# Kernel optimization log

Hardware: AMD Instinct MI355X
Metric: run time of the kernel (lower is better)

## Reference

```python
import jax, jax.numpy as jnp
import numpy as np

HEADS = 16

def setup_inputs() -> dict:
    key = jax.random.key(0)
    k1, k2, k3 = jax.random.split(key, 3)
    B, S, D = 2, 2048, 1024
    return {
        "query": jax.random.normal(k1, (B, S, D), dtype=jnp.float32),
        "key": jax.random.normal(k2, (B, S, D), dtype=jnp.float32),
        "value": jax.random.normal(k3, (B, S, D), dtype=jnp.float32),
    }

def reference(query, key, value):
    B, S, D = query.shape
    H = HEADS
    dh = D // H
    # split(-1) into H equal chunks == reshape to (B, S, H, dh)
    q = query.reshape(B, S, H, dh)
    k = key.reshape(B, S, H, dh)
    v = value.reshape(B, S, H, dh)
    scale = 1.0 / jnp.sqrt(jnp.asarray(dh, dtype=query.dtype))
    scores = jnp.einsum('bqhd,bkhd->bhqk', q, k) * scale  # [B,H,S,S]
    probs = jax.nn.softmax(scores, axis=-1)
    out = jnp.einsum('bhqk,bkhd->bqhd', probs, v)  # [B,S,H,dh]
    return out.reshape(B, S, D)
```

## Files before the change

### kernel.cpp

```cpp
#include <hip/hip_runtime.h>
#include <stdint.h>


#define B_ 2
#define S_ 2048
#define D_ 1024
#define H_ 16
#define DH 64
#define M_TILE 128
#define N_TILE 128
#define NITER (S_ / N_TILE)

typedef __bf16 bf16;
typedef __bf16 bf16x2 __attribute__((ext_vector_type(2)));
typedef __bf16 bf16x4 __attribute__((ext_vector_type(4)));
typedef __bf16 bf16x8 __attribute__((ext_vector_type(8)));
typedef float floatx4 __attribute__((ext_vector_type(4)));

#define KB_TOTAL (B_ * S_ * D_ * 2)
#define KROW_B (D_ * 2)
#define KB_HEAD (S_ * DH * 2)
#define VT_ROW (S_ * 2)
#define WS_NEEDED (2u * KB_TOTAL)

#define N_TILE2 64
#define NITER2 (S_ / N_TILE2)
#define KT2 8192
#define BUF2 16384
#define LSH_OFF2 (4 * BUF2)
#define SMEM_MAIN (LSH_OFF2 + 512)
#define O_STRIDE 36

__device__ __forceinline__ float fast_exp2(float x) {
#if __has_builtin(__builtin_amdgcn_exp2f)
  return __builtin_amdgcn_exp2f(x);
#else
  return exp2f(x);
#endif
}

__device__ __forceinline__ void gl_lds16(const void* g, void* l) {
  __builtin_amdgcn_global_load_lds(
      (const __attribute__((address_space(1))) unsigned int*)g,
      (__attribute__((address_space(3))) unsigned int*)l, 16, 0, 0);
}

__global__ __launch_bounds__(256)
void prep(const float* __restrict__ Kg, const float* __restrict__ Vg,
          unsigned char* __restrict__ ws) {
  const int bid = blockIdx.x;
  const int tid = threadIdx.x;
  if (bid < 512) {
    __shared__ __align__(16) bf16 VTsh[64][136];
    const int head_lin = bid & 31, ktile = bid >> 5;
    const int b = head_lin >> 4, h = head_lin & 15;
    const int kb = ktile * 128;
    const int vr0 = (tid >> 3) << 2;
    const int vf0 = (tid & 7) << 3;
    const float* Vbase = Vg + (size_t)(b * S_) * D_ + h * DH;
    float vals[4][8];
#pragma unroll
    for (int rr = 0; rr < 4; ++rr) {
      const float* vp = Vbase + (size_t)(kb + vr0 + rr) * D_ + vf0;
      float4 a = *(const float4*)vp;
      float4 c = *(const float4*)(vp + 4);
      vals[rr][0] = a.x; vals[rr][1] = a.y; vals[rr][2] = a.z; vals[rr][3] = a.w;
      vals[rr][4] = c.x; vals[rr][5] = c.y; vals[rr][6] = c.z; vals[rr][7] = c.w;
    }
    const int pbase = (vr0 & 96) + ((vr0 >> 2) & 3) * 8 + ((vr0 >> 4) & 1) * 4;
    const int psw = (((pbase >> 3) ^ (tid & 7)) << 3) | (pbase & 7);
#pragma unroll
    for (int j = 0; j < 8; ++j) {
      bf16x4 y = {(bf16)vals[0][j], (bf16)vals[1][j], (bf16)vals[2][j], (bf16)vals[3][j]};
      *(bf16x4*)(&VTsh[vf0 + j][psw]) = y;
    }
    __syncthreads();
    unsigned char* Vout = ws + KB_TOTAL + (size_t)head_lin * KB_HEAD;
#pragma unroll
    for (int j = 0; j < 4; ++j) {
      const int id  = j * 256 + tid;
      const int c   = id & 63;
      const int sub = id >> 6;
      const int fg  = sub & 3;
      const int ckl = sub >> 2;
      const int col = c & 15, quad = c >> 4;
      const int f = fg * 16 + col;
      const int g = ckl * 4 + quad;
      const int gs = g ^ ((f >> 3) & 7);
      bf16x8 v = *(const bf16x8*)(&VTsh[f][gs << 3]);
      *(bf16x8*)(Vout + (size_t)f * VT_ROW + kb * 2 + (ckl * 64 + quad * 16)) = v;
    }
  } else {
    const int idx = (bid - 512) * 256 + tid;
    const float* src = Kg + (size_t)idx * 8;
    float4 x0 = ((const float4*)src)[0];
    float4 x1 = ((const float4*)src)[1];
    bf16x8 y = {(bf16)x0.x, (bf16)x0.y, (bf16)x0.z, (bf16)x0.w,
                (bf16)x1.x, (bf16)x1.y, (bf16)x1.z, (bf16)x1.w};
    *(bf16x8*)(ws + (size_t)idx * 16) = y;
  }
}

__global__ __launch_bounds__(512, 4)
void attn_fwd(const float* __restrict__ Qg, const unsigned char* __restrict__ Kb,
              const unsigned char* __restrict__ VT, float* __restrict__ Og) {
  __shared__ __align__(16) unsigned char smem[SMEM_MAIN];
  float* Osh = (float*)smem;
  float* Lsh = (float*)(smem + LSH_OFF2);

  const int tid  = threadIdx.x;
  const int lane = tid & 63;
  const int wave = tid >> 6;
  const int kw   = wave & 1;
  const int qw   = wave >> 1;
  const int col  = lane & 15;
  const int quad = lane >> 4;

  const int bid      = blockIdx.x;
  const int head_lin = bid & 31;
  const int qtile    = bid >> 5;
  const int b        = head_lin >> 4;
  const int h        = head_lin & 15;

  const unsigned char* Khead = Kb + (size_t)(b * S_) * KROW_B + h * (DH * 2);
  const unsigned char* Vhead = VT + (size_t)head_lin * (DH * VT_ROW);

  const float QSCALE = 0.125f * 1.44269504088896340736f;

  bf16x8 Qf[2][2];
#pragma unroll
  for (int qt = 0; qt < 2; ++qt) {
    const float* base = Qg + (size_t)(b * S_ + qtile * M_TILE + qw * 32 + qt * 16 + col) * D_
                        + h * DH + quad * 8;
#pragma unroll
    for (int ks = 0; ks < 2; ++ks) {
      float4 x0 = *(const float4*)(base + ks * 32);
      float4 x1 = *(const float4*)(base + ks * 32 + 4);
      bf16x8 f;
      f[0] = (bf16)(x0.x * QSCALE); f[1] = (bf16)(x0.y * QSCALE);
      f[2] = (bf16)(x0.z * QSCALE); f[3] = (bf16)(x0.w * QSCALE);
      f[4] = (bf16)(x1.x * QSCALE); f[5] = (bf16)(x1.y * QSCALE);
      f[6] = (bf16)(x1.z * QSCALE); f[7] = (bf16)(x1.w * QSCALE);
      Qf[qt][ks] = f;
    }
  }

  floatx4 accO[4][2];
  float l_lane[2] = {0.f, 0.f};
#pragma unroll
  for (int ft = 0; ft < 4; ++ft)
#pragma unroll
    for (int qt = 0; qt < 2; ++qt) accO[ft][qt] = (floatx4)0.f;

  const int sub = lane >> 3;
  const int gx  = ((lane & 7) ^ sub) << 4;

  auto dma_tile2 = [&](int kbk, int bufoff) {
    const int r = (wave << 3) + sub;
    gl_lds16(Khead + (size_t)(kbk + r) * KROW_B + gx,
             smem + bufoff + (wave << 10));
    gl_lds16(Vhead + (size_t)r * VT_ROW + kbk * 2 + gx,
             smem + bufoff + KT2 + (wave << 10));
  };

  const int cq = col & 7;
  const int ka0_off = (kw * 32 + col) * 128 + ((quad ^ cq) << 4);
  const int ka1_off = (kw * 32 + col) * 128 + (((quad | 4) ^ cq) << 4);
  const int va0_off = KT2 + col * 128 + (((kw * 4 + quad) ^ cq) << 4);

  dma_tile2(0, 0);
  dma_tile2(N_TILE2, BUF2);

  bf16x8 Pf[2];

  for (int it = 0; it < NITER2; ++it) {
    if (it + 2 < NITER2) dma_tile2((it + 2) * N_TILE2, ((it + 2) & 3) * BUF2);
    const int bc = (it & 3) * BUF2;
    const int bp = ((it - 1) & 3) * BUF2;

    __builtin_amdgcn_sched_barrier(0);
    if (it + 2 < NITER2)       asm volatile("s_waitcnt vmcnt(4)" ::: "memory");
    else if (it + 2 == NITER2) asm volatile("s_waitcnt vmcnt(2)" ::: "memory");
    else                       asm volatile("s_waitcnt vmcnt(0)" ::: "memory");
    __builtin_amdgcn_s_barrier();
    asm volatile("" ::: "memory");
    __builtin_amdgcn_sched_barrier(0);

    floatx4 accS[2][2];
    __builtin_amdgcn_s_setprio(1);
#pragma unroll
    for (int kt = 0; kt < 2; ++kt) {
      bf16x8 Ka0 = *(const bf16x8*)(smem + bc + ka0_off + kt * 2048);
      bf16x8 Ka1 = *(const bf16x8*)(smem + bc + ka1_off + kt * 2048);
#pragma unroll
      for (int qt = 0; qt < 2; ++qt) {
        floatx4 a = (floatx4)0.f;
        a = __builtin_amdgcn_mfma_f32_16x16x32_bf16(Ka0, Qf[qt][0], a, 0, 0, 0);
        a = __builtin_amdgcn_mfma_f32_16x16x32_bf16(Ka1, Qf[qt][1], a, 0, 0, 0);
        accS[kt][qt] = a;
      }
    }

    if (it > 0) {
#pragma unroll
      for (int ft = 0; ft < 4; ++ft) {
        bf16x8 Va = *(const bf16x8*)(smem + bp + va0_off + ft * 2048);
#pragma unroll
        for (int qt = 0; qt < 2; ++qt)
          accO[ft][qt] = __builtin_amdgcn_mfma_f32_16x16x32_bf16(Va, Pf[qt], accO[ft][qt], 0, 0, 0);
      }
    }
    __builtin_amdgcn_s_setprio(0);

#pragma unroll
    for (int qt = 0; qt < 2; ++qt) {
      float rs = 0.f;
#pragma unroll
      for (int kt = 0; kt < 2; ++kt)
#pragma unroll
        for (int r = 0; r < 4; ++r) {
          float p = fast_exp2(accS[kt][qt][r]);
          accS[kt][qt][r] = p;
          rs += p;
        }
      l_lane[qt] += rs;
    }
#pragma unroll
    for (int qt = 0; qt < 2; ++qt) {
      floatx4 p0 = accS[0][qt], p1 = accS[1][qt];
      bf16x8 f = {(bf16)p0[0], (bf16)p0[1], (bf16)p0[2], (bf16)p0[3],
                  (bf16)p1[0], (bf16)p1[1], (bf16)p1[2], (bf16)p1[3]};
      Pf[qt] = f;
    }

    __builtin_amdgcn_sched_barrier(0);
    asm volatile("" ::: "memory");
    __builtin_amdgcn_s_barrier();
  }

  {
    const int bp = ((NITER2 - 1) & 3) * BUF2;
    __builtin_amdgcn_s_setprio(1);
#pragma unroll
    for (int ft = 0; ft < 4; ++ft) {
      bf16x8 Va = *(const bf16x8*)(smem + bp + va0_off + ft * 2048);
#pragma unroll
      for (int qt = 0; qt < 2; ++qt)
        accO[ft][qt] = __builtin_amdgcn_mfma_f32_16x16x32_bf16(Va, Pf[qt], accO[ft][qt], 0, 0, 0);
    }
    __builtin_amdgcn_s_setprio(0);
  }
  __syncthreads();

  float l_red[2];
#pragma unroll
  for (int qt = 0; qt < 2; ++qt) {
    float s = l_lane[qt];
    s += __shfl_xor(s, 16);
    s += __shfl_xor(s, 32);
    l_red[qt] = s;
  }

  if (kw == 1) {
    float* r = Osh + (qw * 64 + lane) * O_STRIDE;
#pragma unroll
    for (int qt = 0; qt < 2; ++qt)
#pragma unroll
      for (int ft = 0; ft < 4; ++ft)
        *(floatx4*)(r + (qt * 4 + ft) * 4) = accO[ft][qt];
    if (quad == 0) {
#pragma unroll
      for (int qt = 0; qt < 2; ++qt)
        Lsh[qw * 32 + qt * 16 + col] = l_red[qt];
    }
  }
  __syncthreads();

  if (kw == 0) {
    const float* r = Osh + (qw * 64 + lane) * O_STRIDE;
    float rl[2];
#pragma unroll
    for (int qt = 0; qt < 2; ++qt)
      rl[qt] = 1.0f / (l_red[qt] + Lsh[qw * 32 + qt * 16 + col]);
#pragma unroll
    for (int qt = 0; qt < 2; ++qt) {
      const int q = qtile * M_TILE + qw * 32 + qt * 16 + col;
      float* dst = Og + (size_t)(b * S_ + q) * D_ + h * DH + quad * 4;
#pragma unroll
      for (int ft = 0; ft < 4; ++ft) {
        floatx4 o = (accO[ft][qt] + *(const floatx4*)(r + (qt * 4 + ft) * 4)) * rl[qt];
        *(floatx4*)(dst + ft * 16) = o;
      }
    }
  }
}

#define FB_K_STRIDE 68
#define FB_V_STRIDE 132
#define FB_K_BYTES (128 * FB_K_STRIDE * 2)
#define FB_V_BYTES (64 * FB_V_STRIDE * 2)
#define FB_SMEM ((256 * O_STRIDE * 4 + 2048) > (FB_K_BYTES + FB_V_BYTES) ? (256 * O_STRIDE * 4 + 2048) : (FB_K_BYTES + FB_V_BYTES))

__device__ __forceinline__ bf16x8 cat8(bf16x4 a, bf16x4 b) {
  return __builtin_shufflevector(a, b, 0, 1, 2, 3, 4, 5, 6, 7);
}

__global__ __launch_bounds__(512, 4)
void attn_fwd_fb(const float* __restrict__ Qg, const float* __restrict__ Kg,
                 const float* __restrict__ Vg, float* __restrict__ Og) {
  __shared__ __align__(16) unsigned char smem[FB_SMEM];
  bf16*  Ksh = (bf16*)smem;
  bf16*  Vsh = (bf16*)(smem + FB_K_BYTES);
  float* Osh = (float*)smem;
  float* Lsh = (float*)(smem + 256 * O_STRIDE * 4);

  const int tid  = threadIdx.x;
  const int lane = tid & 63;
  const int wave = tid >> 6;
  const int kw   = wave & 1;
  const int qw   = wave >> 1;
  const int col  = lane & 15;
  const int quad = lane >> 4;
  const int bid      = blockIdx.x;
  const int head_lin = bid & 31;
  const int qtile    = bid >> 5;
  const int b        = head_lin >> 4;
  const int h        = head_lin & 15;
  const float QSCALE = 0.125f * 1.44269504088896340736f;

  bf16x8 Qf[2][2];
#pragma unroll
  for (int qt = 0; qt < 2; ++qt) {
    const float* base = Qg + (size_t)(b * S_ + qtile * 128 + qw * 32 + qt * 16 + col) * D_
                        + h * DH + quad * 8;
#pragma unroll
    for (int ks = 0; ks < 2; ++ks) {
      float4 x0 = *(const float4*)(base + ks * 32);
      float4 x1 = *(const float4*)(base + ks * 32 + 4);
      bf16x8 f;
      f[0] = (bf16)(x0.x * QSCALE); f[1] = (bf16)(x0.y * QSCALE);
      f[2] = (bf16)(x0.z * QSCALE); f[3] = (bf16)(x0.w * QSCALE);
      f[4] = (bf16)(x1.x * QSCALE); f[5] = (bf16)(x1.y * QSCALE);
      f[6] = (bf16)(x1.z * QSCALE); f[7] = (bf16)(x1.w * QSCALE);
      Qf[qt][ks] = f;
    }
  }

  floatx4 accO[4][2];
  float l_lane[2] = {0.f, 0.f};
#pragma unroll
  for (int ft = 0; ft < 4; ++ft)
#pragma unroll
    for (int qt = 0; qt < 2; ++qt) accO[ft][qt] = (floatx4)0.f;

  const float* Kbase = Kg + (size_t)(b * S_) * D_ + h * DH;
  const float* Vbase = Vg + (size_t)(b * S_) * D_ + h * DH;
  const int krow0 = tid >> 4;
  const int kf4   = tid & 15;
  const int vk0   = (tid >> 3) * 2;
  const int vf0   = (tid & 7) * 8;

  for (int it = 0; it < NITER; ++it) {
    const int kb = it * 128;
    float4 kx[4];
#pragma unroll
    for (int i = 0; i < 4; ++i)
      kx[i] = *(const float4*)(Kbase + (size_t)(kb + krow0 + 32 * i) * D_ + kf4 * 4);
    float4 va0 = *(const float4*)(Vbase + (size_t)(kb + vk0) * D_ + vf0);
    float4 va1 = *(const float4*)(Vbase + (size_t)(kb + vk0) * D_ + vf0 + 4);
    float4 vb0 = *(const float4*)(Vbase + (size_t)(kb + vk0 + 1) * D_ + vf0);
    float4 vb1 = *(const float4*)(Vbase + (size_t)(kb + vk0 + 1) * D_ + vf0 + 4);
#pragma unroll
    for (int i = 0; i < 4; ++i) {
      bf16x4 y = {(bf16)kx[i].x, (bf16)kx[i].y, (bf16)kx[i].z, (bf16)kx[i].w};
      *(bf16x4*)(Ksh + (krow0 + 32 * i) * FB_K_STRIDE + kf4 * 4) = y;
    }
    {
      float a[8] = {va0.x, va0.y, va0.z, va0.w, va1.x, va1.y, va1.z, va1.w};
      float c[8] = {vb0.x, vb0.y, vb0.z, vb0.w, vb1.x, vb1.y, vb1.z, vb1.w};
#pragma unroll
      for (int j = 0; j < 8; ++j) {
        bf16x2 y = {(bf16)a[j], (bf16)c[j]};
        *(bf16x2*)(Vsh + (vf0 + j) * FB_V_STRIDE + vk0) = y;
      }
    }
    __syncthreads();

    floatx4 accS[4][2];
#pragma unroll
    for (int kt = 0; kt < 4; ++kt) {
      const bf16* kp = Ksh + (kw * 64 + kt * 16 + col) * FB_K_STRIDE + quad * 8;
      bf16x8 Ka0 = cat8(*(const bf16x4*)kp, *(const bf16x4*)(kp + 4));
      bf16x8 Ka1 = cat8(*(const bf16x4*)(kp + 32), *(const bf16x4*)(kp + 36));
#pragma unroll
      for (int qt = 0; qt < 2; ++qt) {
        floatx4 a = (floatx4)0.f;
        a = __builtin_amdgcn_mfma_f32_16x16x32_bf16(Ka0, Qf[qt][0], a, 0, 0, 0);
        a = __builtin_amdgcn_mfma_f32_16x16x32_bf16(Ka1, Qf[qt][1], a, 0, 0, 0);
        accS[kt][qt] = a;
      }
    }
#pragma unroll
    for (int qt = 0; qt < 2; ++qt) {
      float rs = 0.f;
#pragma unroll
      for (int kt = 0; kt < 4; ++kt)
#pragma unroll
        for (int r = 0; r < 4; ++r) {
          float p = fast_exp2(accS[kt][qt][r]);
          accS[kt][qt][r] = p;
          rs += p;
        }
      l_lane[qt] += rs;
    }
#pragma unroll
    for (int c = 0; c < 2; ++c) {
      bf16x8 Pf[2];
#pragma unroll
      for (int qt = 0; qt < 2; ++qt) {
        floatx4 p0 = accS[2 * c][qt], p1 = accS[2 * c + 1][qt];
        bf16x8 f = {(bf16)p0[0], (bf16)p0[1], (bf16)p0[2], (bf16)p0[3],
                    (bf16)p1[0], (bf16)p1[1], (bf16)p1[2], (bf16)p1[3]};
        Pf[qt] = f;
      }
#pragma unroll
      for (int ft = 0; ft < 4; ++ft) {
        const bf16* vp = Vsh + (ft * 16 + col) * FB_V_STRIDE + kw * 64 + 32 * c + quad * 4;
        bf16x8 Va = cat8(*(const bf16x4*)vp, *(const bf16x4*)(vp + 16));
#pragma unroll
        for (int qt = 0; qt < 2; ++qt)
          accO[ft][qt] = __builtin_amdgcn_mfma_f32_16x16x32_bf16(Va, Pf[qt], accO[ft][qt], 0, 0, 0);
      }
    }
    __syncthreads();
  }

  float l_red[2];
#pragma unroll
  for (int qt = 0; qt < 2; ++qt) {
    float s = l_lane[qt];
    s += __shfl_xor(s, 16);
    s += __shfl_xor(s, 32);
    l_red[qt] = s;
  }
  if (kw == 1) {
    float* r = Osh + (qw * 64 + lane) * O_STRIDE;
#pragma unroll
    for (int qt = 0; qt < 2; ++qt)
#pragma unroll
      for (int ft = 0; ft < 4; ++ft)
        *(floatx4*)(r + (qt * 4 + ft) * 4) = accO[ft][qt];
    if (quad == 0) {
#pragma unroll
      for (int qt = 0; qt < 2; ++qt)
        Lsh[qw * 32 + qt * 16 + col] = l_red[qt];
    }
  }
  __syncthreads();
  if (kw == 0) {
    const float* r = Osh + (qw * 64 + lane) * O_STRIDE;
    float rl[2];
#pragma unroll
    for (int qt = 0; qt < 2; ++qt)
      rl[qt] = 1.0f / (l_red[qt] + Lsh[qw * 32 + qt * 16 + col]);
#pragma unroll
    for (int qt = 0; qt < 2; ++qt) {
      const int q = qtile * 128 + qw * 32 + qt * 16 + col;
      float* dst = Og + (size_t)(b * S_ + q) * D_ + h * DH + quad * 4;
#pragma unroll
      for (int ft = 0; ft < 4; ++ft) {
        floatx4 o = (accO[ft][qt] + *(const floatx4*)(r + (qt * 4 + ft) * 4)) * rl[qt];
        *(floatx4*)(dst + ft * 16) = o;
      }
    }
  }
}

extern "C" void kernel_launch(void* const* d_in, const int* in_sizes, int n_in,
                              void* d_out, int out_size, void* d_ws, size_t ws_size,
                              hipStream_t stream) {
  const float* Q = (const float*)d_in[0];
  const float* K = (const float*)d_in[1];
  const float* V = (const float*)d_in[2];
  float* O = (float*)d_out;
  if (ws_size >= WS_NEEDED && d_ws != nullptr) {
    unsigned char* ws = (unsigned char*)d_ws;
    hipLaunchKernelGGL(prep, dim3(2560), dim3(256), 0, stream, K, V, ws);
    hipLaunchKernelGGL(attn_fwd, dim3(B_ * H_ * (S_ / M_TILE)), dim3(512), 0, stream,
                       Q, ws, ws + KB_TOTAL, O);
  } else {
    hipLaunchKernelGGL(attn_fwd_fb, dim3(512), dim3(512), 0, stream, Q, K, V, O);
  }
}
```

Baseline: 128.5 us.

## Load fp32 K directly into LDS and convert in-kernel, drop K prep pass

The separate K fp32-to-bf16 conversion pass is removed from the prep kernel, which now only transposes V. The attention kernel DMAs raw fp32 K rows into LDS, with a swizzle, and converts to bf16 after the LDS read. The pipeline changes from 4 buffers with 2 tiles in flight to 3 larger buffers with 1 tile prefetched. This saves the K write and re-read through the workspace, but each K tile now moves twice the bytes through global memory and LDS, LDS use grows, and prefetch depth shrinks, which may hurt occupancy and latency hiding.

```diff
diff --git a/kernel.cpp b/kernel.cpp
--- a/kernel.cpp
+++ b/kernel.cpp
@@ -17,18 +17,17 @@
 typedef __bf16 bf16x8 __attribute__((ext_vector_type(8)));
 typedef float floatx4 __attribute__((ext_vector_type(4)));
 
-#define KB_TOTAL (B_ * S_ * D_ * 2)
-#define KROW_B (D_ * 2)
 #define KB_HEAD (S_ * DH * 2)
 #define VT_ROW (S_ * 2)
-#define WS_NEEDED (2u * KB_TOTAL)
+#define WS_NEEDED (32u * KB_HEAD)
+#define KROW_RAW 4096
 
 #define N_TILE2 64
 #define NITER2 (S_ / N_TILE2)
-#define KT2 8192
-#define BUF2 16384
-#define LSH_OFF2 (4 * BUF2)
-#define SMEM_MAIN (LSH_OFF2 + 512)
+#define KT3 16384
+#define BUF3 24576
+#define LSH3 (3 * BUF3)
+#define SMEM_MAIN (LSH3 + 512)
 #define O_STRIDE 36
 
 __device__ __forceinline__ float fast_exp2(float x) {
@@ -46,67 +45,56 @@
 }
 
 __global__ __launch_bounds__(256)
-void prep(const float* __restrict__ Kg, const float* __restrict__ Vg,
-          unsigned char* __restrict__ ws) {
+void prep(const float* __restrict__ Vg, unsigned char* __restrict__ ws) {
+  __shared__ __align__(16) bf16 VTsh[64][136];
   const int bid = blockIdx.x;
   const int tid = threadIdx.x;
-  if (bid < 512) {
-    __shared__ __align__(16) bf16 VTsh[64][136];
-    const int head_lin = bid & 31, ktile = bid >> 5;
-    const int b = head_lin >> 4, h = head_lin & 15;
-    const int kb = ktile * 128;
-    const int vr0 = (tid >> 3) << 2;
-    const int vf0 = (tid & 7) << 3;
-    const float* Vbase = Vg + (size_t)(b * S_) * D_ + h * DH;
-    float vals[4][8];
-#pragma unroll
-    for (int rr = 0; rr < 4; ++rr) {
-      const float* vp = Vbase + (size_t)(kb + vr0 + rr) * D_ + vf0;
-      float4 a = *(const float4*)vp;
-      float4 c = *(const float4*)(vp + 4);
-      vals[rr][0] = a.x; vals[rr][1] = a.y; vals[rr][2] = a.z; vals[rr][3] = a.w;
-      vals[rr][4] = c.x; vals[rr][5] = c.y; vals[rr][6] = c.z; vals[rr][7] = c.w;
-    }
-    const int pbase = (vr0 & 96) + ((vr0 >> 2) & 3) * 8 + ((vr0 >> 4) & 1) * 4;
-    const int psw = (((pbase >> 3) ^ (tid & 7)) << 3) | (pbase & 7);
-#pragma unroll
-    for (int j = 0; j < 8; ++j) {
-      bf16x4 y = {(bf16)vals[0][j], (bf16)vals[1][j], (bf16)vals[2][j], (bf16)vals[3][j]};
-      *(bf16x4*)(&VTsh[vf0 + j][psw]) = y;
-    }
-    __syncthreads();
-    unsigned char* Vout = ws + KB_TOTAL + (size_t)head_lin * KB_HEAD;
-#pragma unroll
-    for (int j = 0; j < 4; ++j) {
-      const int id  = j * 256 + tid;
-      const int c   = id & 63;
-      const int sub = id >> 6;
-      const int fg  = sub & 3;
-      const int ckl = sub >> 2;
-      const int col = c & 15, quad = c >> 4;
-      const int f = fg * 16 + col;
-      const int g = ckl * 4 + quad;
-      const int gs = g ^ ((f >> 3) & 7);
-      bf16x8 v = *(const bf16x8*)(&VTsh[f][gs << 3]);
-      *(bf16x8*)(Vout + (size_t)f * VT_ROW + kb * 2 + (ckl * 64 + quad * 16)) = v;
-    }
-  } else {
-    const int idx = (bid - 512) * 256 + tid;
-    const float* src = Kg + (size_t)idx * 8;
-    float4 x0 = ((const float4*)src)[0];
-    float4 x1 = ((const float4*)src)[1];
-    bf16x8 y = {(bf16)x0.x, (bf16)x0.y, (bf16)x0.z, (bf16)x0.w,
-                (bf16)x1.x, (bf16)x1.y, (bf16)x1.z, (bf16)x1.w};
-    *(bf16x8*)(ws + (size_t)idx * 16) = y;
+  const int head_lin = bid & 31, ktile = bid >> 5;
+  const int b = head_lin >> 4, h = head_lin & 15;
+  const int kb = ktile * 128;
+  const int vr0 = (tid >> 3) << 2;
+  const int vf0 = (tid & 7) << 3;
+  const float* Vbase = Vg + (size_t)(b * S_) * D_ + h * DH;
+  float vals[4][8];
+#pragma unroll
+  for (int rr = 0; rr < 4; ++rr) {
+    const float* vp = Vbase + (size_t)(kb + vr0 + rr) * D_ + vf0;
+    float4 a = *(const float4*)vp;
+    float4 c = *(const float4*)(vp + 4);
+    vals[rr][0] = a.x; vals[rr][1] = a.y; vals[rr][2] = a.z; vals[rr][3] = a.w;
+    vals[rr][4] = c.x; vals[rr][5] = c.y; vals[rr][6] = c.z; vals[rr][7] = c.w;
+  }
+  const int pbase = (vr0 & 96) + ((vr0 >> 2) & 3) * 8 + ((vr0 >> 4) & 1) * 4;
+  const int psw = (((pbase >> 3) ^ (tid & 7)) << 3) | (pbase & 7);
+#pragma unroll
+  for (int j = 0; j < 8; ++j) {
+    bf16x4 y = {(bf16)vals[0][j], (bf16)vals[1][j], (bf16)vals[2][j], (bf16)vals[3][j]};
+    *(bf16x4*)(&VTsh[vf0 + j][psw]) = y;
+  }
+  __syncthreads();
+  unsigned char* Vout = ws + (size_t)head_lin * KB_HEAD;
+#pragma unroll
+  for (int j = 0; j < 4; ++j) {
+    const int id  = j * 256 + tid;
+    const int c   = id & 63;
+    const int sub = id >> 6;
+    const int fg  = sub & 3;
+    const int ckl = sub >> 2;
+    const int col = c & 15, quad = c >> 4;
+    const int f = fg * 16 + col;
+    const int g = ckl * 4 + quad;
+    const int gs = g ^ ((f >> 3) & 7);
+    bf16x8 v = *(const bf16x8*)(&VTsh[f][gs << 3]);
+    *(bf16x8*)(Vout + (size_t)f * VT_ROW + kb * 2 + (ckl * 64 + quad * 16)) = v;
   }
 }
 
 __global__ __launch_bounds__(512, 4)
-void attn_fwd(const float* __restrict__ Qg, const unsigned char* __restrict__ Kb,
+void attn_fwd(const float* __restrict__ Qg, const float* __restrict__ Kg,
               const unsigned char* __restrict__ VT, float* __restrict__ Og) {
   __shared__ __align__(16) unsigned char smem[SMEM_MAIN];
   float* Osh = (float*)smem;
-  float* Lsh = (float*)(smem + LSH_OFF2);
+  float* Lsh = (float*)(smem + LSH3);
 
   const int tid  = threadIdx.x;
   const int lane = tid & 63;
@@ -122,8 +110,8 @@
   const int b        = head_lin >> 4;
   const int h        = head_lin & 15;
 
-  const unsigned char* Khead = Kb + (size_t)(b * S_) * KROW_B + h * (DH * 2);
-  const unsigned char* Vhead = VT + (size_t)head_lin * (DH * VT_ROW);
+  const unsigned char* Kraw = (const unsigned char*)Kg + (size_t)(b * S_) * KROW_RAW + h * 256;
+  const unsigned char* Vhead = VT + (size_t)head_lin * KB_HEAD;
 
   const float QSCALE = 0.125f * 1.44269504088896340736f;
 
@@ -152,36 +140,42 @@
 #pragma unroll
     for (int qt = 0; qt < 2; ++qt) accO[ft][qt] = (floatx4)0.f;
 
-  const int sub = lane >> 3;
-  const int gx  = ((lane & 7) ^ sub) << 4;
-
-  auto dma_tile2 = [&](int kbk, int bufoff) {
-    const int r = (wave << 3) + sub;
-    gl_lds16(Khead + (size_t)(kbk + r) * KROW_B + gx,
-             smem + bufoff + (wave << 10));
-    gl_lds16(Vhead + (size_t)r * VT_ROW + kbk * 2 + gx,
-             smem + bufoff + KT2 + (wave << 10));
+  const int sub   = lane >> 3;
+  const int gx    = ((lane & 7) ^ sub) << 4;
+  const int krloc = lane >> 4;
+  const int kgr   = lane & 15;
+
+  auto dma_tile3 = [&](int kbk, int bufoff) {
+#pragma unroll
+    for (int t = 0; t < 2; ++t) {
+      const int r7 = t * 4 + krloc;
+      gl_lds16(Kraw + (size_t)(kbk + wave * 8 + r7) * KROW_RAW + ((kgr ^ r7) << 4),
+               smem + bufoff + (wave * 8 + t * 4) * 256);
+    }
+    gl_lds16(Vhead + (size_t)(wave * 8 + sub) * VT_ROW + kbk * 2 + gx,
+             smem + bufoff + KT3 + (wave << 10));
   };
 
   const int cq = col & 7;
-  const int ka0_off = (kw * 32 + col) * 128 + ((quad ^ cq) << 4);
-  const int ka1_off = (kw * 32 + col) * 128 + (((quad | 4) ^ cq) << 4);
-  const int va0_off = KT2 + col * 128 + (((kw * 4 + quad) ^ cq) << 4);
-
-  dma_tile2(0, 0);
-  dma_tile2(N_TILE2, BUF2);
+  const int rKb = (kw * 32 + col) * 256;
+  const int a0l = rKb + (((2 * quad)     ^ cq) << 4);
+  const int a0h = rKb + (((2 * quad + 1) ^ cq) << 4);
+  const int a1l = rKb + (((2 * quad + 8) ^ cq) << 4);
+  const int a1h = rKb + (((2 * quad + 9) ^ cq) << 4);
+  const int va0_off = KT3 + col * 128 + (((kw * 4 + quad) ^ cq) << 4);
+
+  dma_tile3(0, 0);
 
   bf16x8 Pf[2];
 
   for (int it = 0; it < NITER2; ++it) {
-    if (it + 2 < NITER2) dma_tile2((it + 2) * N_TILE2, ((it + 2) & 3) * BUF2);
-    const int bc = (it & 3) * BUF2;
-    const int bp = ((it - 1) & 3) * BUF2;
+    if (it + 1 < NITER2) dma_tile3((it + 1) * N_TILE2, ((it + 1) % 3) * BUF3);
+    const int bc = (it % 3) * BUF3;
+    const int bp = ((it + 2) % 3) * BUF3;
 
     __builtin_amdgcn_sched_barrier(0);
-    if (it + 2 < NITER2)       asm volatile("s_waitcnt vmcnt(4)" ::: "memory");
-    else if (it + 2 == NITER2) asm volatile("s_waitcnt vmcnt(2)" ::: "memory");
-    else                       asm volatile("s_waitcnt vmcnt(0)" ::: "memory");
+    if (it + 1 < NITER2) asm volatile("s_waitcnt vmcnt(3)" ::: "memory");
+    else                 asm volatile("s_waitcnt vmcnt(0)" ::: "memory");
     __builtin_amdgcn_s_barrier();
     asm volatile("" ::: "memory");
     __builtin_amdgcn_sched_barrier(0);
@@ -190,8 +184,15 @@
     __builtin_amdgcn_s_setprio(1);
 #pragma unroll
     for (int kt = 0; kt < 2; ++kt) {
-      bf16x8 Ka0 = *(const bf16x8*)(smem + bc + ka0_off + kt * 2048);
-      bf16x8 Ka1 = *(const bf16x8*)(smem + bc + ka1_off + kt * 2048);
+      const unsigned char* kp = smem + bc + kt * 4096;
+      floatx4 l0 = *(const floatx4*)(kp + a0l);
+      floatx4 h0 = *(const floatx4*)(kp + a0h);
+      floatx4 l1 = *(const floatx4*)(kp + a1l);
+      floatx4 h1 = *(const floatx4*)(kp + a1h);
+      bf16x8 Ka0 = {(bf16)l0[0], (bf16)l0[1], (bf16)l0[2], (bf16)l0[3],
+                    (bf16)h0[0], (bf16)h0[1], (bf16)h0[2], (bf16)h0[3]};
+      bf16x8 Ka1 = {(bf16)l1[0], (bf16)l1[1], (bf16)l1[2], (bf16)l1[3],
+                    (bf16)h1[0], (bf16)h1[1], (bf16)h1[2], (bf16)h1[3]};
 #pragma unroll
       for (int qt = 0; qt < 2; ++qt) {
         floatx4 a = (floatx4)0.f;
@@ -239,7 +240,7 @@
   }
 
   {
-    const int bp = ((NITER2 - 1) & 3) * BUF2;
+    const int bp = ((NITER2 - 1) % 3) * BUF3;
     __builtin_amdgcn_s_setprio(1);
 #pragma unroll
     for (int ft = 0; ft < 4; ++ft) {
@@ -485,9 +486,9 @@
   float* O = (float*)d_out;
   if (ws_size >= WS_NEEDED && d_ws != nullptr) {
     unsigned char* ws = (unsigned char*)d_ws;
-    hipLaunchKernelGGL(prep, dim3(2560), dim3(256), 0, stream, K, V, ws);
+    hipLaunchKernelGGL(prep, dim3(512), dim3(256), 0, stream, V, ws);
     hipLaunchKernelGGL(attn_fwd, dim3(B_ * H_ * (S_ / M_TILE)), dim3(512), 0, stream,
-                       Q, ws, ws + KB_TOTAL, O);
+                       Q, K, ws, O);
   } else {
     hipLaunchKernelGGL(attn_fwd_fb, dim3(512), dim3(512), 0, stream, Q, K, V, O);
   }
```

Measured after the change: 132.0 us. 2.7% more time.
